# Performance work log

Measured on AMD Instinct MI355X. Metric: run time of the kernel, lower is better.

The kernel has to match this reference:

```python
import jax, jax.numpy as jnp
import numpy as np

B, H, W = 32, 64, 64
C1, C2, K = 32, 64, 5
FC1 = 512
FLAT = C2 * H * W  # 262144


def setup_inputs() -> dict:
    key = jax.random.key(0)
    ks = jax.random.split(key, 9)
    return {
        "x": jax.random.normal(ks[0], (B, 1, H, W), dtype=jnp.float32),
        "w1r": jax.random.normal(ks[1], (C1, 1, K, K), dtype=jnp.float32),
        "w1i": jax.random.normal(ks[2], (C1, 1, K, K), dtype=jnp.float32),
        "w2r": jax.random.normal(ks[3], (C2, C1, K, K), dtype=jnp.float32),
        "w2i": jax.random.normal(ks[4], (C2, C1, K, K), dtype=jnp.float32),
        "fc1_w": jax.random.normal(ks[5], (FC1, FLAT), dtype=jnp.float32) * 0.01,
        "fc1_b": jax.random.normal(ks[6], (FC1,), dtype=jnp.float32),
        "fc2_w": jax.random.normal(ks[7], (10, FC1), dtype=jnp.float32) * 0.05,
        "fc2_b": jax.random.normal(ks[8], (10,), dtype=jnp.float32),
    }


def freq_conv(x, wr, wi):
    # kernel: (out, in, K, K) complex, zero-padded to (out, in, H, W), FFT2'd once
    # (the torch code redundantly tiles this per batch; math is identical)
    kern = wr + 1j * wi  # complex64
    h, w = x.shape[-2], x.shape[-1]
    kern_pad = jnp.pad(kern, ((0, 0), (0, 0), (0, h - K), (0, w - K)))
    kf = jnp.fft.fft2(kern_pad)  # (out, in, H, W) complex64
    # fused multiply + sum over in_channels: (B,in,H,W) x (out,in,H,W) -> (B,out,H,W)
    return jnp.einsum("bihw,oihw->bohw", x.astype(jnp.complex64), kf)


def reference(x, w1r, w1i, w2r, w2i, fc1_w, fc1_b, fc2_w, fc2_b):
    h1 = jnp.abs(freq_conv(x, w1r, w1i))          # (B, C1, H, W) float32
    h2 = jnp.abs(freq_conv(h1, w2r, w2i))         # (B, C2, H, W) float32
    flat = h2.reshape(h2.shape[0], -1)            # (B, FLAT)
    y = flat @ fc1_w.T + fc1_b                    # (B, FC1)
    return y @ fc2_w.T + fc2_b                    # (B, 10)
```

## Files before the change

kernel.cpp:

```cpp
#include <hip/hip_runtime.h>
#include <math.h>

#define PI2 6.283185307179586f

typedef float floatx4 __attribute__((ext_vector_type(4)));


__global__ void kA_small(const float* __restrict__ w1r, const float* __restrict__ w1i,
                         const float* __restrict__ w2r, const float* __restrict__ w2i,
                         float* __restrict__ a1, float* __restrict__ G_re,
                         float* __restrict__ G_im) {
    if (blockIdx.x < 512) {
        int idx = blockIdx.x * 256 + threadIdx.x;
        int i  = idx >> 12;
        int hw = idx & 4095;
        int u = hw >> 6, v = hw & 63;
        const float* wr = w1r + i * 25;
        const float* wi = w1i + i * 25;
        float re = 0.f, im = 0.f;
        #pragma unroll
        for (int p = 0; p < 5; ++p) {
            #pragma unroll
            for (int q = 0; q < 5; ++q) {
                float s, c;
                sincosf(-(PI2 / 64.f) * (float)((u * p + v * q) & 63), &s, &c);
                float ar = wr[p * 5 + q], ai = wi[p * 5 + q];
                re += ar * c - ai * s;
                im += ar * s + ai * c;
            }
        }
        a1[idx] = sqrtf(re * re + im * im);
    } else {
        int idx = (blockIdx.x - 512) * 256 + threadIdx.x;
        int v  = idx & 63;
        int p  = (idx >> 6) % 5;
        int oi = idx / 320;
        const float* wr = w2r + oi * 25 + p * 5;
        const float* wi = w2i + oi * 25 + p * 5;
        float re = 0.f, im = 0.f;
        #pragma unroll
        for (int q = 0; q < 5; ++q) {
            float s, c;
            sincosf(-(PI2 / 64.f) * (float)((v * q) & 63), &s, &c);
            re += wr[q] * c - wi[q] * s;
            im += wr[q] * s + wi[q] * c;
        }
        G_re[idx] = re;
        G_im[idx] = im;
    }
}

__global__ void k2b_t(const float* __restrict__ G_re, const float* __restrict__ G_im,
                      const float* __restrict__ a1, float* __restrict__ t) {
    __shared__ float Gsr[5120];
    __shared__ float Gsi[5120];
    int o  = blockIdx.x >> 2;
    int ug = blockIdx.x & 3;
    float re[4] = {0.f, 0.f, 0.f, 0.f};
    float im[4] = {0.f, 0.f, 0.f, 0.f};
    for (int half = 0; half < 2; ++half) {
        __syncthreads();
        for (int jj = threadIdx.x; jj < 5120; jj += 256) {
            Gsr[jj] = G_re[o * 10240 + half * 5120 + jj];
            Gsi[jj] = G_im[o * 10240 + half * 5120 + jj];
        }
        __syncthreads();
        #pragma unroll
        for (int jt = 0; jt < 4; ++jt) {
            int j = jt * 256 + threadIdx.x;
            int u = ug * 16 + (j >> 6);
            int v = j & 63;
            float cu[5], su[5];
            #pragma unroll
            for (int p = 0; p < 5; ++p)
                sincosf(-(PI2 / 64.f) * (float)((u * p) & 63), &su[p], &cu[p]);
            #pragma unroll 4
            for (int i = 0; i < 16; ++i) {
                float a = a1[(half * 16 + i) * 4096 + u * 64 + v];
                float sr = 0.f, si = 0.f;
                #pragma unroll
                for (int p = 0; p < 5; ++p) {
                    float gr = Gsr[(i * 5 + p) * 64 + v];
                    float gi = Gsi[(i * 5 + p) * 64 + v];
                    sr += gr * cu[p] - gi * su[p];
                    si += gr * su[p] + gi * cu[p];
                }
                re[jt] += a * sr;
                im[jt] += a * si;
            }
        }
    }
    #pragma unroll
    for (int jt = 0; jt < 4; ++jt) {
        int j = jt * 256 + threadIdx.x;
        int u = ug * 16 + (j >> 6);
        int v = j & 63;
        t[o * 4096 + u * 64 + v] = sqrtf(re[jt] * re[jt] + im[jt] * im[jt]);
    }
}

__global__ __launch_bounds__(256) void k3_y1(
        const float* __restrict__ fc1_w, const float* __restrict__ t,
        const float* __restrict__ x, float* __restrict__ y1) {
    int f0 = (blockIdx.x >> 2) * 2;
    int hb = blockIdx.x & 3;
    int hw = hb * 1024 + threadIdx.x * 4;
    const floatx4* w0 = (const floatx4*)(fc1_w + (size_t)f0 * 262144);
    const floatx4* w1 = (const floatx4*)(fc1_w + (size_t)(f0 + 1) * 262144);
    floatx4 acc0 = (floatx4)(0.f);
    floatx4 acc1 = (floatx4)(0.f);
    #pragma unroll 8
    for (int o = 0; o < 64; ++o) {
        int e = (o * 4096 + hw) >> 2;
        floatx4 tv = *(const floatx4*)(t + o * 4096 + hw);
        floatx4 wa = __builtin_nontemporal_load(w0 + e);
        floatx4 wb = __builtin_nontemporal_load(w1 + e);
        acc0 += tv * wa;
        acc1 += tv * wb;
    }
    __shared__ float red[4][32][2];
    int wave = threadIdx.x >> 6;
    int lane = threadIdx.x & 63;
    for (int b = 0; b < 32; ++b) {
        floatx4 xv = *(const floatx4*)(x + b * 4096 + hw);
        float ax = fabsf(xv.x), ay = fabsf(xv.y), az = fabsf(xv.z), aw = fabsf(xv.w);
        float p0 = acc0.x * ax + acc0.y * ay + acc0.z * az + acc0.w * aw;
        float p1 = acc1.x * ax + acc1.y * ay + acc1.z * az + acc1.w * aw;
        #pragma unroll
        for (int m = 32; m >= 1; m >>= 1) {
            p0 += __shfl_xor(p0, m, 64);
            p1 += __shfl_xor(p1, m, 64);
        }
        if (lane == 0) { red[wave][b][0] = p0; red[wave][b][1] = p1; }
    }
    __syncthreads();
    if (threadIdx.x < 64) {
        int b = threadIdx.x >> 1, ff = threadIdx.x & 1;
        float s = red[0][b][ff] + red[1][b][ff] + red[2][b][ff] + red[3][b][ff];
        atomicAdd(&y1[b * 512 + f0 + ff], s);
    }
}

__global__ void k4_out(const float* __restrict__ y1, const float* __restrict__ fc1_b,
                       const float* __restrict__ fc2_w, const float* __restrict__ fc2_b,
                       float* __restrict__ out) {
    int tid = threadIdx.x;
    if (tid >= 320) return;
    int b = tid / 10, c = tid % 10;
    float acc = fc2_b[c];
    for (int f = 0; f < 512; ++f)
        acc += fc2_w[c * 512 + f] * (y1[b * 512 + f] + fc1_b[f]);
    out[b * 10 + c] = acc;
}

extern "C" void kernel_launch(void* const* d_in, const int* in_sizes, int n_in,
                              void* d_out, int out_size, void* d_ws, size_t ws_size,
                              hipStream_t stream) {
    const float* x    = (const float*)d_in[0];
    const float* w1r  = (const float*)d_in[1];
    const float* w1i  = (const float*)d_in[2];
    const float* w2r  = (const float*)d_in[3];
    const float* w2i  = (const float*)d_in[4];
    const float* fc1w = (const float*)d_in[5];
    const float* fc1b = (const float*)d_in[6];
    const float* fc2w = (const float*)d_in[7];
    const float* fc2b = (const float*)d_in[8];
    float* out = (float*)d_out;

    float* a1   = (float*)d_ws;
    float* G_re = a1 + 131072;
    float* G_im = G_re + 655360;
    float* t    = G_im + 655360;
    float* y1   = t + 262144;

    (void)hipMemsetAsync(y1, 0, 16384 * sizeof(float), stream);
    kA_small<<<3072, 256, 0, stream>>>(w1r, w1i, w2r, w2i, a1, G_re, G_im);
    k2b_t<<<256, 256, 0, stream>>>(G_re, G_im, a1, t);
    k3_y1<<<1024, 256, 0, stream>>>(fc1w, t, x, y1);
    k4_out<<<1, 320, 0, stream>>>(y1, fc1b, fc2w, fc2b, out);
}
```

Baseline: 771.4 us.

## Split conv kernel across more blocks, use twiddle table, parallelize final FC

The second-layer frequency conv kernel now uses 8 row groups per output channel instead of 4, doubling the block count to fill more compute units. It reads its per-row twiddle factors from a small shared-memory table rather than calling sincosf. The final FC2 kernel is restructured from one block with long serial loops into one wave per batch row with shuffle reductions, and the FC1 loop unroll is raised. Each block reloads the same G slice, so duplicated G loads increase.

```diff
diff --git a/kernel.cpp b/kernel.cpp
--- a/kernel.cpp
+++ b/kernel.cpp
@@ -50,14 +50,23 @@
     }
 }
 
-__global__ void k2b_t(const float* __restrict__ G_re, const float* __restrict__ G_im,
-                      const float* __restrict__ a1, float* __restrict__ t) {
+__global__ __launch_bounds__(256) void k2b_t(
+        const float* __restrict__ G_re, const float* __restrict__ G_im,
+        const float* __restrict__ a1, float* __restrict__ t) {
     __shared__ float Gsr[5120];
     __shared__ float Gsi[5120];
-    int o  = blockIdx.x >> 2;
-    int ug = blockIdx.x & 3;
-    float re[4] = {0.f, 0.f, 0.f, 0.f};
-    float im[4] = {0.f, 0.f, 0.f, 0.f};
+    __shared__ float twc[64];
+    __shared__ float tws[64];
+    int o  = blockIdx.x >> 3;
+    int ug = blockIdx.x & 7;
+    if (threadIdx.x < 64) {
+        float s, c;
+        sincosf(-(PI2 / 64.f) * (float)threadIdx.x, &s, &c);
+        twc[threadIdx.x] = c;
+        tws[threadIdx.x] = s;
+    }
+    float re[2] = {0.f, 0.f};
+    float im[2] = {0.f, 0.f};
     for (int half = 0; half < 2; ++half) {
         __syncthreads();
         for (int jj = threadIdx.x; jj < 5120; jj += 256) {
@@ -66,14 +75,17 @@
         }
         __syncthreads();
         #pragma unroll
-        for (int jt = 0; jt < 4; ++jt) {
+        for (int jt = 0; jt < 2; ++jt) {
             int j = jt * 256 + threadIdx.x;
-            int u = ug * 16 + (j >> 6);
+            int u = ug * 8 + (j >> 6);
             int v = j & 63;
             float cu[5], su[5];
             #pragma unroll
-            for (int p = 0; p < 5; ++p)
-                sincosf(-(PI2 / 64.f) * (float)((u * p) & 63), &su[p], &cu[p]);
+            for (int p = 0; p < 5; ++p) {
+                int k = (u * p) & 63;
+                cu[p] = twc[k];
+                su[p] = tws[k];
+            }
             #pragma unroll 4
             for (int i = 0; i < 16; ++i) {
                 float a = a1[(half * 16 + i) * 4096 + u * 64 + v];
@@ -91,9 +103,9 @@
         }
     }
     #pragma unroll
-    for (int jt = 0; jt < 4; ++jt) {
+    for (int jt = 0; jt < 2; ++jt) {
         int j = jt * 256 + threadIdx.x;
-        int u = ug * 16 + (j >> 6);
+        int u = ug * 8 + (j >> 6);
         int v = j & 63;
         t[o * 4096 + u * 64 + v] = sqrtf(re[jt] * re[jt] + im[jt] * im[jt]);
     }
@@ -109,7 +121,7 @@
     const floatx4* w1 = (const floatx4*)(fc1_w + (size_t)(f0 + 1) * 262144);
     floatx4 acc0 = (floatx4)(0.f);
     floatx4 acc1 = (floatx4)(0.f);
-    #pragma unroll 8
+    #pragma unroll 16
     for (int o = 0; o < 64; ++o) {
         int e = (o * 4096 + hw) >> 2;
         floatx4 tv = *(const floatx4*)(t + o * 4096 + hw);
@@ -141,16 +153,34 @@
     }
 }
 
-__global__ void k4_out(const float* __restrict__ y1, const float* __restrict__ fc1_b,
-                       const float* __restrict__ fc2_w, const float* __restrict__ fc2_b,
-                       float* __restrict__ out) {
-    int tid = threadIdx.x;
-    if (tid >= 320) return;
-    int b = tid / 10, c = tid % 10;
-    float acc = fc2_b[c];
-    for (int f = 0; f < 512; ++f)
-        acc += fc2_w[c * 512 + f] * (y1[b * 512 + f] + fc1_b[f]);
-    out[b * 10 + c] = acc;
+__global__ __launch_bounds__(64) void k4_out(
+        const float* __restrict__ y1, const float* __restrict__ fc1_b,
+        const float* __restrict__ fc2_w, const float* __restrict__ fc2_b,
+        float* __restrict__ out) {
+    int b = blockIdx.x;
+    int lane = threadIdx.x;
+    float acc[10];
+    #pragma unroll
+    for (int c = 0; c < 10; ++c) acc[c] = 0.f;
+    #pragma unroll
+    for (int k = 0; k < 8; ++k) {
+        int f = k * 64 + lane;
+        float v = y1[b * 512 + f] + fc1_b[f];
+        #pragma unroll
+        for (int c = 0; c < 10; ++c)
+            acc[c] += fc2_w[c * 512 + f] * v;
+    }
+    #pragma unroll
+    for (int c = 0; c < 10; ++c) {
+        #pragma unroll
+        for (int m = 32; m >= 1; m >>= 1)
+            acc[c] += __shfl_xor(acc[c], m, 64);
+    }
+    if (lane == 0) {
+        #pragma unroll
+        for (int c = 0; c < 10; ++c)
+            out[b * 10 + c] = acc[c] + fc2_b[c];
+    }
 }
 
 extern "C" void kernel_launch(void* const* d_in, const int* in_sizes, int n_in,
@@ -175,7 +205,7 @@
 
     (void)hipMemsetAsync(y1, 0, 16384 * sizeof(float), stream);
     kA_small<<<3072, 256, 0, stream>>>(w1r, w1i, w2r, w2i, a1, G_re, G_im);
-    k2b_t<<<256, 256, 0, stream>>>(G_re, G_im, a1, t);
+    k2b_t<<<512, 256, 0, stream>>>(G_re, G_im, a1, t);
     k3_y1<<<1024, 256, 0, stream>>>(fc1w, t, x, y1);
-    k4_out<<<1, 320, 0, stream>>>(y1, fc1b, fc2w, fc2b, out);
-}
+    k4_out<<<32, 64, 0, stream>>>(y1, fc1b, fc2w, fc2b, out);
+}
```

Result: faster. 717.6 us (-7.0%).
